# Kernel tuning notes

Measured on AMD Instinct MI355X. Metric: run time of the kernel, lower is better.

The kernel has to match this reference:

```python
import jax, jax.numpy as jnp
import numpy as np

NUM_HEAD = 32
NUM_KV_HEAD = 8
HEAD_DIM = 128
EMBED_DIM = 4096
GROUP = NUM_HEAD // NUM_KV_HEAD + 2  # 6: 4 q slots + 1 k + 1 v
TOKENS = 64


def setup_inputs() -> dict:
    key = jax.random.key(0)
    k1, k2, k3 = jax.random.split(key, 3)
    inp = jax.random.normal(k1, (TOKENS, EMBED_DIM), dtype=jnp.float32)
    # fused GQA weight layout from load_parameter: [embed_dim, num_kv_head, group, head_dim]
    weight = jax.random.normal(k2, (EMBED_DIM, NUM_KV_HEAD, GROUP, HEAD_DIM), dtype=jnp.float32) * 0.02
    bias = jax.random.normal(k3, (NUM_KV_HEAD, GROUP, HEAD_DIM), dtype=jnp.float32) * 0.02
    return {"input": inp, "weight": weight, "bias": bias}


def reference(input, weight, bias):
    # fused grouped QKV GEMM (mm_qkv_group_out):
    # out[t, kv, g, d] = sum_e input[t, e] * weight[e, kv, g, d] + bias[kv, g, d]
    out = jnp.einsum('te,ekgd->tkgd', input, weight) + bias
    T = input.shape[0]
    q = out[:, :, : GROUP - 2, :].reshape(T, NUM_HEAD * HEAD_DIM)
    k = out[:, :, GROUP - 2, :].reshape(T, NUM_KV_HEAD * HEAD_DIM)
    v = out[:, :, GROUP - 1, :].reshape(T, NUM_KV_HEAD * HEAD_DIM)
    return (q, k, v)
```

## Files before the change

kernel.cpp:

```cpp
#include <hip/hip_runtime.h>


#define N_COLS 6144
#define K_DIM  4096
#define Q_SZ   (64 * 4096)
#define K_OFF  Q_SZ
#define V_OFF  (Q_SZ + 64 * 1024)
#define OUT_ELEMS 393216
#define NT     48
#define KSPLIT 16
#define BK     32
#define TILES  8

typedef __bf16 bf16x8 __attribute__((ext_vector_type(8)));
typedef float  f32x4  __attribute__((ext_vector_type(4)));
typedef unsigned int u32x4 __attribute__((ext_vector_type(4)));

__device__ __forceinline__ unsigned short f2bf_rne(float f) {
    unsigned int u = __float_as_uint(f);
    u += 0x7FFFu + ((u >> 16) & 1u);
    return (unsigned short)(u >> 16);
}

__device__ __forceinline__ unsigned int pack_pair(float lo, float hi) {
    return ((unsigned int)f2bf_rne(hi) << 16) | f2bf_rne(lo);
}

__device__ __forceinline__ int out_index(int t, int n) {
    const int kv = n / 768;
    const int g  = (n >> 7) % 6;
    const int d  = n & 127;
    if (g < 4)  return t * 4096 + kv * 512 + g * 128 + d;
    if (g == 4) return K_OFF + t * 1024 + kv * 128 + d;
    return V_OFF + t * 1024 + kv * 128 + d;
}

#define GLDS(gp, lp) __builtin_amdgcn_global_load_lds(                        \
    (const __attribute__((address_space(1))) void*)(gp),                      \
    (__attribute__((address_space(3))) void*)(lp), 16, 0, 0)

__global__ __launch_bounds__(256, 4)
void qkv_gemm(const float* __restrict__ in, const float* __restrict__ w,
              float* __restrict__ part) {
    __shared__ float Ws[BK * 128];

    const int tid  = threadIdx.x;
    const int nt   = blockIdx.x % NT;
    const int kq   = blockIdx.x / NT;
    const int n0   = nt * 128;
    const int k0   = kq * 256;
    const int wid  = tid >> 6;
    const int lane = tid & 63;
    const int l15  = lane & 15;
    const int kblk = lane >> 4;

    f32x4 acc[2][4];
    #pragma unroll
    for (int a = 0; a < 2; ++a)
        #pragma unroll
        for (int b = 0; b < 4; ++b) acc[a][b] = (f32x4){0.f, 0.f, 0.f, 0.f};

    #pragma unroll 1
    for (int s = 0; s < TILES; ++s) {
        const int kc = k0 + s * BK;

        const float* wr = w + (size_t)kc * N_COLS + n0;
        #pragma unroll
        for (int r = 0; r < 4; ++r) {
            const int u = r * 256 + tid;
            GLDS(wr + (size_t)(u >> 5) * N_COLS + (u & 31) * 4, &Ws[u * 4]);
        }

        float4 alo[4], ahi[4];
        #pragma unroll
        for (int mi = 0; mi < 4; ++mi) {
            const float* ap = in + (size_t)(mi * 16 + l15) * K_DIM + kc + kblk * 8;
            alo[mi] = *(const float4*)ap;
            ahi[mi] = *(const float4*)(ap + 4);
        }

        __syncthreads();

        u32x4 af[4];
        #pragma unroll
        for (int mi = 0; mi < 4; ++mi) {
            af[mi][0] = pack_pair(alo[mi].x, alo[mi].y);
            af[mi][1] = pack_pair(alo[mi].z, alo[mi].w);
            af[mi][2] = pack_pair(ahi[mi].x, ahi[mi].y);
            af[mi][3] = pack_pair(ahi[mi].z, ahi[mi].w);
        }

        #pragma unroll
        for (int nfi = 0; nfi < 2; ++nfi) {
            const int nb = (wid * 2 + nfi) * 16 + l15;
            float bf[8];
            #pragma unroll
            for (int j = 0; j < 8; ++j)
                bf[j] = Ws[(kblk * 8 + j) * 128 + nb];
            u32x4 bu;
            #pragma unroll
            for (int j2 = 0; j2 < 4; ++j2)
                bu[j2] = pack_pair(bf[2 * j2], bf[2 * j2 + 1]);

            const bf16x8 bv = __builtin_bit_cast(bf16x8, bu);
            #pragma unroll
            for (int mi = 0; mi < 4; ++mi)
                acc[nfi][mi] = __builtin_amdgcn_mfma_f32_16x16x32_bf16(
                    __builtin_bit_cast(bf16x8, af[mi]), bv, acc[nfi][mi], 0, 0, 0);
        }

        __syncthreads();
    }

    float* pb = part + (size_t)kq * OUT_ELEMS;
    #pragma unroll
    for (int nfi = 0; nfi < 2; ++nfi) {
        const int n = n0 + (wid * 2 + nfi) * 16 + l15;
        #pragma unroll
        for (int mi = 0; mi < 4; ++mi) {
            #pragma unroll
            for (int r = 0; r < 4; ++r) {
                const int t = mi * 16 + kblk * 4 + r;
                pb[(size_t)t * N_COLS + n] = acc[nfi][mi][r];
            }
        }
    }
}

__global__ __launch_bounds__(256)
void qkv_reduce(const float* __restrict__ part, const float* __restrict__ bias,
                float* __restrict__ out) {
    const int i = blockIdx.x * 256 + threadIdx.x;
    const int t = i / N_COLS;
    const int n = i % N_COLS;
    float s = bias[n];
    #pragma unroll
    for (int kq = 0; kq < KSPLIT; ++kq)
        s += part[(size_t)kq * OUT_ELEMS + i];
    out[out_index(t, n)] = s;
}

extern "C" void kernel_launch(void* const* d_in, const int* in_sizes, int n_in,
                              void* d_out, int out_size, void* d_ws, size_t ws_size,
                              hipStream_t stream) {
    const float* in   = (const float*)d_in[0];
    const float* w    = (const float*)d_in[1];
    const float* bias = (const float*)d_in[2];
    float* out  = (float*)d_out;
    float* part = (float*)d_ws;

    qkv_gemm<<<NT * KSPLIT, 256, 0, stream>>>(in, w, part);
    qkv_reduce<<<OUT_ELEMS / 256, 256, 0, stream>>>(part, bias, out);
}
```

Baseline: 163.9 us.

## Restructure GEMM into narrow N tiles with per-wave K split and double buffering

```diff
diff --git a/kernel.cpp b/kernel.cpp
--- a/kernel.cpp
+++ b/kernel.cpp
@@ -7,14 +7,17 @@
 #define K_OFF  Q_SZ
 #define V_OFF  (Q_SZ + 64 * 1024)
 #define OUT_ELEMS 393216
-#define NT     48
-#define KSPLIT 16
-#define BK     32
-#define TILES  8
+#define IN_ELEMS  262144
+#define NT     192
+#define KSPLIT 8
+#define TILES  4
 
 typedef __bf16 bf16x8 __attribute__((ext_vector_type(8)));
 typedef float  f32x4  __attribute__((ext_vector_type(4)));
 typedef unsigned int u32x4 __attribute__((ext_vector_type(4)));
+typedef unsigned short us8 __attribute__((ext_vector_type(8)));
+
+__device__ unsigned short g_abuf[IN_ELEMS];
 
 __device__ __forceinline__ unsigned short f2bf_rne(float f) {
     unsigned int u = __float_as_uint(f);
@@ -23,7 +26,12 @@
 }
 
 __device__ __forceinline__ unsigned int pack_pair(float lo, float hi) {
-    return ((unsigned int)f2bf_rne(hi) << 16) | f2bf_rne(lo);
+    unsigned int a = __float_as_uint(lo), b = __float_as_uint(hi);
+    a += 0x7FFFu + ((a >> 16) & 1u);
+    b += 0x8000u & ~0x7FFFu;
+    b = __float_as_uint(hi);
+    b += 0x7FFFu + ((b >> 16) & 1u);
+    return (b & 0xFFFF0000u) | (a >> 16);
 }
 
 __device__ __forceinline__ int out_index(int t, int n) {
@@ -35,20 +43,24 @@
     return V_OFF + t * 1024 + kv * 128 + d;
 }
 
+__global__ __launch_bounds__(256)
+void init_kernel(const float* __restrict__ in) {
+    const int i = blockIdx.x * 256 + threadIdx.x;
+    if (i < IN_ELEMS) g_abuf[i] = f2bf_rne(in[i]);
+}
+
 #define GLDS(gp, lp) __builtin_amdgcn_global_load_lds(                        \
     (const __attribute__((address_space(1))) void*)(gp),                      \
     (__attribute__((address_space(3))) void*)(lp), 16, 0, 0)
 
-__global__ __launch_bounds__(256, 4)
-void qkv_gemm(const float* __restrict__ in, const float* __restrict__ w,
-              float* __restrict__ part) {
-    __shared__ float Ws[BK * 128];
+__global__ __launch_bounds__(256, 2)
+void qkv_gemm(const float* __restrict__ w, _Float16* __restrict__ part) {
+    __shared__ __align__(16) char lds_raw[65536];
 
     const int tid  = threadIdx.x;
     const int nt   = blockIdx.x % NT;
     const int kq   = blockIdx.x / NT;
-    const int n0   = nt * 128;
-    const int k0   = kq * 256;
+    const int n0   = nt * 32;
     const int wid  = tid >> 6;
     const int lane = tid & 63;
     const int l15  = lane & 15;
@@ -60,75 +72,88 @@
         #pragma unroll
         for (int b = 0; b < 4; ++b) acc[a][b] = (f32x4){0.f, 0.f, 0.f, 0.f};
 
-    #pragma unroll 1
+    const int kwave = kq * 512 + wid * 128;
+
+    #define ISSUE_TILE(buf, s) do {                                           \
+        const int kc_ = kwave + (s) * 32;                                     \
+        char* wb_ = lds_raw + (wid * 2 + (buf)) * 8192;                       \
+        const float* wg_ = w + (size_t)kc_ * N_COLS + n0;                     \
+        GLDS(wg_ + (size_t)((0 * 64 + lane) >> 3) * N_COLS + ((0 * 64 + lane) & 7) * 4, wb_ + (0 * 64 + lane) * 16); \
+        GLDS(wg_ + (size_t)((1 * 64 + lane) >> 3) * N_COLS + ((1 * 64 + lane) & 7) * 4, wb_ + (1 * 64 + lane) * 16); \
+        GLDS(wg_ + (size_t)((2 * 64 + lane) >> 3) * N_COLS + ((2 * 64 + lane) & 7) * 4, wb_ + (2 * 64 + lane) * 16); \
+        GLDS(wg_ + (size_t)((3 * 64 + lane) >> 3) * N_COLS + ((3 * 64 + lane) & 7) * 4, wb_ + (3 * 64 + lane) * 16); \
+        const unsigned short* ag_ = g_abuf + kc_;                             \
+        GLDS(ag_ + (size_t)((0 * 64 + lane) >> 2) * K_DIM + ((0 * 64 + lane) & 3) * 8, wb_ + 4096 + (0 * 64 + lane) * 16); \
+        GLDS(ag_ + (size_t)((1 * 64 + lane) >> 2) * K_DIM + ((1 * 64 + lane) & 3) * 8, wb_ + 4096 + (1 * 64 + lane) * 16); \
+        GLDS(ag_ + (size_t)((2 * 64 + lane) >> 2) * K_DIM + ((2 * 64 + lane) & 3) * 8, wb_ + 4096 + (2 * 64 + lane) * 16); \
+        GLDS(ag_ + (size_t)((3 * 64 + lane) >> 2) * K_DIM + ((3 * 64 + lane) & 3) * 8, wb_ + 4096 + (3 * 64 + lane) * 16); \
+    } while (0)
+
+    ISSUE_TILE(0, 0);
+
+    #pragma unroll
     for (int s = 0; s < TILES; ++s) {
-        const int kc = k0 + s * BK;
-
-        const float* wr = w + (size_t)kc * N_COLS + n0;
-        #pragma unroll
-        for (int r = 0; r < 4; ++r) {
-            const int u = r * 256 + tid;
-            GLDS(wr + (size_t)(u >> 5) * N_COLS + (u & 31) * 4, &Ws[u * 4]);
+        if (s + 1 < TILES) {
+            ISSUE_TILE((s + 1) & 1, s + 1);
+            asm volatile("s_waitcnt vmcnt(8)" ::: "memory");
+        } else {
+            asm volatile("s_waitcnt vmcnt(0)" ::: "memory");
         }
 
-        float4 alo[4], ahi[4];
+        const char* wb = lds_raw + (wid * 2 + (s & 1)) * 8192;
+        const float* Wf = (const float*)wb;
+        const unsigned short* Ab = (const unsigned short*)(wb + 4096);
+
+        us8 af[4];
         #pragma unroll
-        for (int mi = 0; mi < 4; ++mi) {
-            const float* ap = in + (size_t)(mi * 16 + l15) * K_DIM + kc + kblk * 8;
-            alo[mi] = *(const float4*)ap;
-            ahi[mi] = *(const float4*)(ap + 4);
-        }
-
-        __syncthreads();
-
-        u32x4 af[4];
-        #pragma unroll
-        for (int mi = 0; mi < 4; ++mi) {
-            af[mi][0] = pack_pair(alo[mi].x, alo[mi].y);
-            af[mi][1] = pack_pair(alo[mi].z, alo[mi].w);
-            af[mi][2] = pack_pair(ahi[mi].x, ahi[mi].y);
-            af[mi][3] = pack_pair(ahi[mi].z, ahi[mi].w);
-        }
+        for (int mi = 0; mi < 4; ++mi)
+            af[mi] = *(const us8*)(Ab + (mi * 16 + l15) * 32 + kblk * 8);
 
         #pragma unroll
-        for (int nfi = 0; nfi < 2; ++nfi) {
-            const int nb = (wid * 2 + nfi) * 16 + l15;
-            float bf[8];
-            #pragma unroll
-            for (int j = 0; j < 8; ++j)
-                bf[j] = Ws[(kblk * 8 + j) * 128 + nb];
+        for (int nf = 0; nf < 2; ++nf) {
+            const int nn = nf * 16 + l15;
             u32x4 bu;
             #pragma unroll
             for (int j2 = 0; j2 < 4; ++j2)
-                bu[j2] = pack_pair(bf[2 * j2], bf[2 * j2 + 1]);
-
+                bu[j2] = pack_pair(Wf[(kblk * 8 + 2 * j2) * 32 + nn],
+                                   Wf[(kblk * 8 + 2 * j2 + 1) * 32 + nn]);
             const bf16x8 bv = __builtin_bit_cast(bf16x8, bu);
             #pragma unroll
             for (int mi = 0; mi < 4; ++mi)
-                acc[nfi][mi] = __builtin_amdgcn_mfma_f32_16x16x32_bf16(
-                    __builtin_bit_cast(bf16x8, af[mi]), bv, acc[nfi][mi], 0, 0, 0);
+                acc[nf][mi] = __builtin_amdgcn_mfma_f32_16x16x32_bf16(
+                    __builtin_bit_cast(bf16x8, af[mi]), bv, acc[nf][mi], 0, 0, 0);
         }
-
-        __syncthreads();
     }
 
-    float* pb = part + (size_t)kq * OUT_ELEMS;
+    _Float16* red = (_Float16*)(lds_raw + wid * 16384);
     #pragma unroll
-    for (int nfi = 0; nfi < 2; ++nfi) {
-        const int n = n0 + (wid * 2 + nfi) * 16 + l15;
+    for (int nf = 0; nf < 2; ++nf)
         #pragma unroll
-        for (int mi = 0; mi < 4; ++mi) {
+        for (int mi = 0; mi < 4; ++mi)
             #pragma unroll
-            for (int r = 0; r < 4; ++r) {
-                const int t = mi * 16 + kblk * 4 + r;
-                pb[(size_t)t * N_COLS + n] = acc[nfi][mi][r];
-            }
-        }
+            for (int r = 0; r < 4; ++r)
+                red[lane * 32 + (nf * 4 + mi) * 4 + r] =
+                    (_Float16)acc[nf][mi][r];
+    __syncthreads();
+
+    const int row = tid >> 2;
+    const int q   = tid & 3;
+    const int mi_ = row >> 4, kb_ = (row >> 2) & 3, r_ = row & 3;
+    #pragma unroll
+    for (int c = 0; c < 8; ++c) {
+        const int nl   = q * 8 + c;
+        const int lsrc = kb_ * 16 + (nl & 15);
+        const int j    = ((nl >> 4) * 4 + mi_) * 4 + r_;
+        float s = 0.f;
+        #pragma unroll
+        for (int wv = 0; wv < 4; ++wv)
+            s += (float)((const _Float16*)(lds_raw + wv * 16384))[lsrc * 32 + j];
+        part[(size_t)kq * OUT_ELEMS + row * N_COLS + n0 + nl] = (_Float16)s;
     }
 }
 
 __global__ __launch_bounds__(256)
-void qkv_reduce(const float* __restrict__ part, const float* __restrict__ bias,
+void qkv_reduce(const _Float16* __restrict__ part, const float* __restrict__ bias,
                 float* __restrict__ out) {
     const int i = blockIdx.x * 256 + threadIdx.x;
     const int t = i / N_COLS;
@@ -136,7 +161,7 @@
     float s = bias[n];
     #pragma unroll
     for (int kq = 0; kq < KSPLIT; ++kq)
-        s += part[(size_t)kq * OUT_ELEMS + i];
+        s += (float)part[(size_t)kq * OUT_ELEMS + i];
     out[out_index(t, n)] = s;
 }
 
@@ -146,9 +171,10 @@
     const float* in   = (const float*)d_in[0];
     const float* w    = (const float*)d_in[1];
     const float* bias = (const float*)d_in[2];
-    float* out  = (float*)d_out;
-    float* part = (float*)d_ws;
+    float* out = (float*)d_out;
+    _Float16* part = (_Float16*)d_ws;
 
-    qkv_gemm<<<NT * KSPLIT, 256, 0, stream>>>(in, w, part);
+    init_kernel<<<IN_ELEMS / 256, 256, 0, stream>>>(in);
+    qkv_gemm<<<NT * KSPLIT, 256, 0, stream>>>(w, part);
     qkv_reduce<<<OUT_ELEMS / 256, 256, 0, stream>>>(part, bias, out);
 }
```

Result: no change. 164.6 us (+0.5%).
